# Kernel optimization log

Hardware: AMD Instinct MI355X
Metric: run time of the kernel (lower is better)

## Reference

```python
import jax, jax.numpy as jnp
import numpy as np

NV, NK, DK, DV, KC = 32, 16, 128, 128, 4  # value heads, key heads, head dims, conv kernel
EPS = 1e-6


def setup_inputs() -> dict:
    key = jax.random.key(0)
    ks = jax.random.split(key, 10)
    B, T, D = 2, 4096, 2048
    key_dim, value_dim = NK * DK, NV * DV
    conv_dim = 2 * key_dim + value_dim
    s = 0.02
    return {
        "hidden_states": jax.random.normal(ks[0], (B, T, D), jnp.float32),
        "W_qkv": jax.random.normal(ks[1], (D, conv_dim), jnp.float32) * s,
        "W_z": jax.random.normal(ks[2], (D, value_dim), jnp.float32) * s,
        "W_b": jax.random.normal(ks[3], (D, NV), jnp.float32) * s,
        "W_a": jax.random.normal(ks[4], (D, NV), jnp.float32) * s,
        "conv_w": jax.random.normal(ks[5], (conv_dim, KC), jnp.float32) * 0.2,
        "dt_bias": jnp.ones((NV,), jnp.float32),
        "A_log": jnp.log(jax.random.uniform(ks[6], (NV,), jnp.float32, 0.5, 16.0)),
        "norm_w": jnp.ones((DV,), jnp.float32),
        "W_out": jax.random.normal(ks[7], (value_dim, D), jnp.float32) * s,
    }


def _silu(x):
    return x * jax.nn.sigmoid(x)


def _l2norm(x):
    return x * jax.lax.rsqrt(jnp.sum(x * x, axis=-1, keepdims=True) + EPS)


def _gated_delta_rule(q, k, v, g, beta):
    # q,k: [B,T,H,DK]; v: [B,T,H,DV]; g,beta: [B,T,H]
    tm = lambda x: jnp.moveaxis(x, 1, 0)  # time-major
    B, T, H = q.shape[0], q.shape[1], q.shape[2]
    S0 = jnp.zeros((B, H, q.shape[-1], v.shape[-1]), q.dtype)

    def step(S, xs):
        qt, kt, vt, gt, bt = xs
        S = S * jnp.exp(gt)[..., None, None]                       # decay
        kS = jnp.einsum('bhk,bhkv->bhv', kt, S)                    # k^T S
        S = S + bt[..., None, None] * kt[..., :, None] * (vt - kS)[..., None, :]
        o = jnp.einsum('bhk,bhkv->bhv', qt, S)
        return S, o

    _, o = jax.lax.scan(step, S0, (tm(q), tm(k), tm(v), tm(g), tm(beta)))
    return jnp.moveaxis(o, 0, 1)  # [B,T,H,DV]


def reference(hidden_states, W_qkv, W_z, W_b, W_a, conv_w, dt_bias, A_log, norm_w, W_out):
    B, T, D = hidden_states.shape
    key_dim, value_dim = NK * DK, NV * DV

    mixed = hidden_states @ W_qkv                                  # [B,T,conv_dim]
    z = (hidden_states @ W_z).reshape(B, T, NV, DV)
    beta = jax.nn.sigmoid(hidden_states @ W_b)                     # [B,T,NV]
    a = hidden_states @ W_a
    g = -jnp.exp(A_log) * jax.nn.softplus(a + dt_bias)             # [B,T,NV]

    # causal depthwise short conv (kernel KC) + silu
    xp = jnp.pad(mixed, ((0, 0), (KC - 1, 0), (0, 0)))
    conv = sum(xp[:, i:i + T, :] * conv_w[:, i] for i in range(KC))
    mixed = _silu(conv)

    q, k, v = jnp.split(mixed, [key_dim, 2 * key_dim], axis=-1)
    q = q.reshape(B, T, NK, DK)
    k = k.reshape(B, T, NK, DK)
    v = v.reshape(B, T, NV, DV)
    rep = NV // NK
    q = jnp.repeat(q, rep, axis=2)
    k = jnp.repeat(k, rep, axis=2)

    q = _l2norm(q) * (DK ** -0.5)
    k = _l2norm(k)

    o = _gated_delta_rule(q, k, v, g, beta)                        # [B,T,NV,DV]

    # fused gated RMSNorm: rmsnorm(o)*w * silu(z)
    var = jnp.mean(o * o, axis=-1, keepdims=True)
    o = o * jax.lax.rsqrt(var + 1e-6) * norm_w * _silu(z)

    return o.reshape(B, T, value_dim) @ W_out
```

## Files before the change

### kernel.cpp

```cpp
#include <hip/hip_runtime.h>
#include <hip/hip_bf16.h>


typedef __attribute__((ext_vector_type(8))) short short8;
typedef __attribute__((ext_vector_type(4))) float f32x4;
typedef unsigned short us;

static __device__ __forceinline__ us f2b(float f) {
  __hip_bfloat16 h = __float2bfloat16(f);
  return __builtin_bit_cast(us, h);
}
static __device__ __forceinline__ float b2f(us u) {
  return __bfloat162float(__builtin_bit_cast(__hip_bfloat16, u));
}

__global__ __launch_bounds__(256) void cvt_f32_bf16(const float* __restrict__ in,
    us* __restrict__ out, long n4) {
  long i = (long)blockIdx.x * 256 + threadIdx.x;
  long stride = (long)gridDim.x * 256;
  for (; i < n4; i += stride) {
    float4 f = reinterpret_cast<const float4*>(in)[i];
    ushort4 u;
    u.x = f2b(f.x); u.y = f2b(f.y); u.z = f2b(f.z); u.w = f2b(f.w);
    reinterpret_cast<ushort4*>(out)[i] = u;
  }
}

__global__ __launch_bounds__(256) void transpose_cvt(const float* __restrict__ in,
    us* __restrict__ out, int K, int N, int Nfull, int coloff, int row_off) {
  __shared__ float tile[64][65];
  int tid = threadIdx.x;
  int n0 = blockIdx.x * 64, k0 = blockIdx.y * 64;
  int tx = tid & 15, ty = tid >> 4;
#pragma unroll
  for (int r = 0; r < 4; ++r) {
    int kk = k0 + ty + r * 16, nn = n0 + tx * 4;
    float4 v = make_float4(0.f, 0.f, 0.f, 0.f);
    if (kk < K && nn < N)
      v = *reinterpret_cast<const float4*>(in + (size_t)kk * Nfull + coloff + nn);
    tile[ty + r * 16][tx * 4 + 0] = v.x;
    tile[ty + r * 16][tx * 4 + 1] = v.y;
    tile[ty + r * 16][tx * 4 + 2] = v.z;
    tile[ty + r * 16][tx * 4 + 3] = v.w;
  }
  __syncthreads();
#pragma unroll
  for (int g = 0; g < 2; ++g) {
    int s = tid + g * 256;
    int nn = s >> 3, ks = (s & 7) * 8;
    if (n0 + nn < N && k0 + ks < K) {
      us ov[8];
#pragma unroll
      for (int i = 0; i < 8; ++i) ov[i] = f2b(tile[ks + i][nn]);
      *reinterpret_cast<uint4*>(out + (size_t)(n0 + nn + row_off) * K + k0 + ks) =
          *reinterpret_cast<uint4*>(ov);
    }
  }
}

template <bool BF16OUT>
__global__ __launch_bounds__(512, 1) void gemm256(const us* __restrict__ A,
    const us* __restrict__ B, void* __restrict__ Cout, int K, int ldC) {
  __shared__ us Abuf[2][256 * 64];
  __shared__ us Bbuf[2][256 * 64];
  int tid = threadIdx.x, w = tid >> 6, lane = tid & 63;
  int wr = w >> 2, wc = w & 3;
  int fr = lane & 15, j4 = lane >> 4;
  int lin = blockIdx.y * gridDim.x + blockIdx.x;
  int nwg = gridDim.x * gridDim.y;
  int wg = (lin & 7) * (nwg >> 3) + (lin >> 3);
  int bx = wg % gridDim.x, by = wg / gridDim.x;
  size_t bm = (size_t)bx * 256, bn = (size_t)by * 256;

  const us *aG[4], *bG[4];
  us *aL[2][4], *bL[2][4];
#pragma unroll
  for (int u = 0; u < 4; ++u) {
    int idx = u * 512 + tid;
    int row = idx >> 3, sl = idx & 7;
    int sg = (sl ^ (row & 7)) * 8;
    aG[u] = A + (bm + row) * K + sg;
    bG[u] = B + (bn + row) * K + sg;
    int lbase = (u * 64 + w * 8) * 64;
#pragma unroll
    for (int bf = 0; bf < 2; ++bf) {
      aL[bf][u] = &Abuf[bf][lbase];
      bL[bf][u] = &Bbuf[bf][lbase];
    }
  }

  f32x4 acc[8][4] = {};
#pragma unroll
  for (int u = 0; u < 4; ++u) {
    __builtin_amdgcn_global_load_lds((const void*)aG[u], (void*)aL[0][u], 16, 0, 0);
    __builtin_amdgcn_global_load_lds((const void*)bG[u], (void*)bL[0][u], 16, 0, 0);
  }
  __syncthreads();

  int nt = K >> 6;
  for (int t = 0; t < nt; ++t) {
    int cur = t & 1, nxt = cur ^ 1;
    const us* Ac = Abuf[cur];
    const us* Bc = Bbuf[cur];
    int kt1 = (t + 1) << 6;
    bool more = (t + 1 < nt);
#pragma unroll
    for (int q = 0; q < 4; ++q) {
      if (more) {
        __builtin_amdgcn_global_load_lds((const void*)(aG[q] + kt1), (void*)aL[nxt][q], 16, 0, 0);
        __builtin_amdgcn_global_load_lds((const void*)(bG[q] + kt1), (void*)bL[nxt][q], 16, 0, 0);
      }
      short8 a0[2], a1[2], bfv[4][2];
      int Ra0 = wr * 128 + 2 * q * 16 + fr;
      int Ra1 = Ra0 + 16;
#pragma unroll
      for (int ks = 0; ks < 2; ++ks) {
        a0[ks] = *reinterpret_cast<const short8*>(&Ac[Ra0 * 64 + (((ks * 4 + j4) ^ (Ra0 & 7)) * 8)]);
        a1[ks] = *reinterpret_cast<const short8*>(&Ac[Ra1 * 64 + (((ks * 4 + j4) ^ (Ra1 & 7)) * 8)]);
#pragma unroll
        for (int fj = 0; fj < 4; ++fj) {
          int Rb = wc * 64 + fj * 16 + fr;
          bfv[fj][ks] = *reinterpret_cast<const short8*>(&Bc[Rb * 64 + (((ks * 4 + j4) ^ (Rb & 7)) * 8)]);
        }
      }
      __builtin_amdgcn_s_setprio(1);
#pragma unroll
      for (int ks = 0; ks < 2; ++ks)
#pragma unroll
        for (int fj = 0; fj < 4; ++fj) {
          acc[2 * q][fj] = __builtin_amdgcn_mfma_f32_16x16x32_bf16(a0[ks], bfv[fj][ks], acc[2 * q][fj], 0, 0, 0);
          acc[2 * q + 1][fj] = __builtin_amdgcn_mfma_f32_16x16x32_bf16(a1[ks], bfv[fj][ks], acc[2 * q + 1][fj], 0, 0, 0);
        }
      __builtin_amdgcn_s_setprio(0);
    }
    __syncthreads();
  }
#pragma unroll
  for (int fi = 0; fi < 8; ++fi)
#pragma unroll
    for (int fj = 0; fj < 4; ++fj) {
      size_t col = bn + wc * 64 + fj * 16 + fr;
#pragma unroll
      for (int e = 0; e < 4; ++e) {
        size_t r = bm + wr * 128 + fi * 16 + j4 * 4 + e;
        size_t off = r * ldC + col;
        if (BF16OUT) reinterpret_cast<us*>(Cout)[off] = f2b(acc[fi][fj][e]);
        else reinterpret_cast<float*>(Cout)[off] = acc[fi][fj][e];
      }
    }
}

__global__ __launch_bounds__(256) void gemm_lds_f32(const us* __restrict__ A,
    const us* __restrict__ B, float* __restrict__ Cout,
    int K, int Nb1, int Nvalid, int ldC) {
  __shared__ us Ash[128 * 64];
  __shared__ us Bsh[128 * 64];
  int tid = threadIdx.x, w = tid >> 6, lane = tid & 63;
  int bm = blockIdx.x * 128, bn = blockIdx.y * 128;
  int wm = (w >> 1) * 64, wn = (w & 1) * 64;
  const us* aP[4]; const us* bP[4]; us* lA[4]; us* lB[4];
#pragma unroll
  for (int i = 0; i < 4; ++i) {
    int idx = i * 256 + tid;
    int row = idx >> 3;
    int sg = ((idx & 7) ^ (row & 7)) * 8;
    aP[i] = A + (size_t)(bm + row) * K + sg;
    int rb = bn + row; if (rb > Nb1) rb = Nb1;
    bP[i] = B + (size_t)rb * K + sg;
    lA[i] = &Ash[(i * 256 + w * 64) * 8];
    lB[i] = &Bsh[(i * 256 + w * 64) * 8];
  }
  f32x4 acc[4][4] = {};
  int fr = lane & 15, j = lane >> 4;
  for (int kt = 0; kt < K; kt += 64) {
#pragma unroll
    for (int i = 0; i < 4; ++i)
      __builtin_amdgcn_global_load_lds((const void*)(aP[i] + kt), (void*)lA[i], 16, 0, 0);
#pragma unroll
    for (int i = 0; i < 4; ++i)
      __builtin_amdgcn_global_load_lds((const void*)(bP[i] + kt), (void*)lB[i], 16, 0, 0);
    __syncthreads();
#pragma unroll
    for (int ks = 0; ks < 2; ++ks) {
      short8 af[4], bfr[4];
#pragma unroll
      for (int f = 0; f < 4; ++f) {
        int Ra = wm + f * 16 + fr;
        af[f] = *reinterpret_cast<const short8*>(&Ash[Ra * 64 + (((ks * 4 + j) ^ (Ra & 7)) * 8)]);
        int Rb = wn + f * 16 + fr;
        bfr[f] = *reinterpret_cast<const short8*>(&Bsh[Rb * 64 + (((ks * 4 + j) ^ (Rb & 7)) * 8)]);
      }
#pragma unroll
      for (int i = 0; i < 4; ++i)
#pragma unroll
        for (int jj = 0; jj < 4; ++jj)
          acc[i][jj] = __builtin_amdgcn_mfma_f32_16x16x32_bf16(af[i], bfr[jj], acc[i][jj], 0, 0, 0);
    }
    __syncthreads();
  }
#pragma unroll
  for (int i = 0; i < 4; ++i)
#pragma unroll
    for (int jj = 0; jj < 4; ++jj) {
      int c0 = bn + wn + jj * 16 + (lane & 15);
      if (c0 < Nvalid) {
#pragma unroll
        for (int e = 0; e < 4; ++e) {
          int r = bm + wm + i * 16 + (lane >> 4) * 4 + e;
          Cout[(size_t)r * ldC + c0] = acc[i][jj][e];
        }
      }
    }
}

template <int MODE>
__global__ __launch_bounds__(256) void conv_chunk(const us* __restrict__ mixed,
    const float* __restrict__ cw, us* __restrict__ outp, int headbase) {
  int bt = blockIdx.x, b = bt >> 12, t = bt & 4095, tid = threadIdx.x;
  int c0 = tid * 8;
  float wv[8][4];
#pragma unroll
  for (int jj = 0; jj < 8; ++jj) {
    float4 w4 = *reinterpret_cast<const float4*>(cw + (size_t)(c0 + jj) * 4);
    wv[jj][0] = w4.x; wv[jj][1] = w4.y; wv[jj][2] = w4.z; wv[jj][3] = w4.w;
  }
  float acc[8] = {};
#pragma unroll
  for (int i = 0; i < 4; ++i) {
    int tt = t - 3 + i;
    if (tt >= 0) {
      us r[8];
      *reinterpret_cast<uint4*>(r) = *reinterpret_cast<const uint4*>(
          mixed + ((size_t)(b * 4096 + tt)) * 2048 + c0);
#pragma unroll
      for (int jj = 0; jj < 8; ++jj) acc[jj] += b2f(r[jj]) * wv[jj][i];
    }
  }
  float x[8];
#pragma unroll
  for (int jj = 0; jj < 8; ++jj) x[jj] = acc[jj] / (1.f + __expf(-acc[jj]));
  us ov[8];
  if (MODE < 2) {
    float s2 = 0.f;
#pragma unroll
    for (int jj = 0; jj < 8; ++jj) s2 += x[jj] * x[jj];
#pragma unroll
    for (int m = 1; m < 16; m <<= 1) s2 += __shfl_xor(s2, m, 64);
    float rn = rsqrtf(s2 + 1e-6f) * (MODE == 0 ? 0.08838834764831845f : 1.f);
#pragma unroll
    for (int jj = 0; jj < 8; ++jj) ov[jj] = f2b(x[jj] * rn);
    int head = tid >> 4, d0 = c0 & 127;
    *reinterpret_cast<uint4*>(outp + ((size_t)bt * 16 + head) * 128 + d0) =
        *reinterpret_cast<uint4*>(ov);
  } else {
#pragma unroll
    for (int jj = 0; jj < 8; ++jj) ov[jj] = f2b(x[jj]);
    *reinterpret_cast<uint4*>(outp + ((size_t)bt * 32 + headbase + (c0 >> 7)) * 128 + (c0 & 127)) =
        *reinterpret_cast<uint4*>(ov);
  }
}

__global__ __launch_bounds__(256) void gates_cumsum(const float* __restrict__ ba,
    const float* __restrict__ dt_bias, const float* __restrict__ A_log,
    float* __restrict__ bl_g, float* __restrict__ beta_g) {
  int widx = blockIdx.x * 4 + (threadIdx.x >> 6);
  int lane = threadIdx.x & 63;
  int bh = widx >> 6, chunk = widx & 63;
  int b = bh >> 5, h = bh & 31;
  size_t btl = (size_t)b * 4096 + chunk * 64 + lane;
  float bv = ba[btl * 64 + h];
  float av = ba[btl * 64 + 32 + h];
  float beta = 1.f / (1.f + __expf(-bv));
  float xx = av + dt_bias[h];
  float sp = (xx > 20.f) ? xx : log1pf(__expf(xx));
  float g = -__expf(A_log[h]) * sp;
#pragma unroll
  for (int off = 1; off < 64; off <<= 1) {
    float n = __shfl_up(g, off, 64);
    if (lane >= off) g += n;
  }
  bl_g[(size_t)widx * 64 + lane] = g;
  beta_g[(size_t)widx * 64 + lane] = beta;
}

static __device__ __forceinline__ f32x4 tile_range(const us* A, int lda,
    const us* B, int ldb, int rt, int ct, int l0, int nk, int lane, f32x4 acc) {
  const us* ar = A + (rt * 16 + (lane & 15)) * lda + l0 * 16 + (lane >> 4) * 8;
  const us* br = B + (ct * 16 + (lane & 15)) * ldb + l0 * 16 + (lane >> 4) * 8;
#pragma unroll
  for (int ks = 0; ks < nk; ++ks) {
    short8 a = *reinterpret_cast<const short8*>(ar + ks * 32);
    short8 bb = *reinterpret_cast<const short8*>(br + ks * 32);
    acc = __builtin_amdgcn_mfma_f32_16x16x32_bf16(a, bb, acc, 0, 0, 0);
  }
  return acc;
}

__global__ __launch_bounds__(512, 1) void scan_p1(
    const us* __restrict__ k, const float* __restrict__ bl_g,
    const float* __restrict__ beta_g, us* __restrict__ Tg) {
  __shared__ us Kb[64 * 136];
  __shared__ us Ebt[64 * 72];
  __shared__ us W1[64 * 72], W1t[64 * 72], W3[64 * 72];
  __shared__ float bl_s[64], bet_s[64];
  us* const Eb = Kb;

  int bid = blockIdx.x, bh = bid >> 6, c = bid & 63;
  int b = bh >> 5, h = bh & 31, hk = h >> 1;
  int tid = threadIdx.x, w = tid >> 6, lane = tid & 63;
  int row = tid >> 3, c16 = (tid & 7) * 16;
  size_t bt0 = (size_t)b * 4096 + c * 64;

  const int TR_[10] = {0, 1, 1, 2, 2, 2, 3, 3, 3, 3};
  const int TC_[10] = {0, 0, 1, 0, 1, 2, 0, 1, 2, 3};

  const us* kp = k + ((bt0 + row) * 16 + hk) * 128 + c16;
  uint4 kr0 = reinterpret_cast<const uint4*>(kp)[0];
  uint4 kr1 = reinterpret_cast<const uint4*>(kp)[1];
  int gbase = (bh * 64 + c) * 64;
  if (tid < 64) { bl_s[tid] = bl_g[gbase + tid]; bet_s[tid] = beta_g[gbase + tid]; }
  *reinterpret_cast<uint4*>(&Kb[row * 136 + c16]) = kr0;
  *reinterpret_cast<uint4*>(&Kb[row * 136 + c16 + 8]) = kr1;
  __syncthreads();
  {
    int art = w & 3;
#pragma unroll
    for (int s = 0; s < 2; ++s) {
      int ct = (w >> 2) * 2 + s;
      f32x4 a = tile_range(Kb, 136, Kb, 136, art, ct, 0, 4, lane, f32x4{});
#pragma unroll
      for (int e = 0; e < 4; ++e) {
        int tr = art * 16 + (lane >> 4) * 4 + e;
        int cl = ct * 16 + (lane & 15);
        float dv = (cl < tr) ? bet_s[tr] * __expf(bl_s[tr] - bl_s[cl]) * a[e] : 0.f;
        W1[tr * 72 + cl] = f2b(dv);
        W1t[cl * 72 + tr] = f2b(dv);
        W3[tr * 72 + cl] = f2b((tr == cl ? 1.f : 0.f) - dv);
      }
    }
  }
  __syncthreads();
  f32x4 freg[2] = {};
#pragma unroll
  for (int it = 1; it <= 5; ++it) {
    if (it > 1) {
#pragma unroll
      for (int s = 0; s < 2; ++s) {
        int j = w + s * 8;
        if (j < 10) {
          int r = TR_[j], cc0 = TC_[j];
#pragma unroll
          for (int e = 0; e < 4; ++e) {
            int rr = r * 16 + (lane >> 4) * 4 + e, cl = cc0 * 16 + (lane & 15);
            W3[rr * 72 + cl] = f2b(b2f(W3[rr * 72 + cl]) + freg[s][e]);
          }
        }
      }
    }
    if (it == 1) {
      const int ZR[12] = {0, 0, 0, 1, 1, 2, 1, 2, 2, 3, 3, 3};
      const int ZC[12] = {1, 2, 3, 2, 3, 3, 0, 0, 1, 0, 1, 2};
#pragma unroll
      for (int u = 0; u < 12; ++u) {
        if ((u & 7) != w) continue;
        us* arr = (u < 6) ? Eb : Ebt;
        if (lane < 32) {
          int rr = ZR[u] * 16 + (lane >> 1);
          *reinterpret_cast<uint4*>(&arr[rr * 72 + ZC[u] * 16 + (lane & 1) * 8]) =
              make_uint4(0, 0, 0, 0);
        }
      }
    }
    const us* Es  = (it & 1) ? W1  : Eb;
    const us* Est = (it & 1) ? W1t : Ebt;
    us* Ed  = (it & 1) ? Eb  : W1;
    us* Edt = (it & 1) ? Ebt : W1t;
#pragma unroll
    for (int s = 0; s < 2; ++s) {
      int j = w + s * 8;
      if (j < 10) {
        int r = TR_[j], cc0 = TC_[j];
        int l0 = cc0 & ~1, nk = (r - l0 + 2) >> 1;
        f32x4 a = tile_range(Es, 72, Est, 72, r, cc0, l0, nk, lane, f32x4{});
#pragma unroll
        for (int e = 0; e < 4; ++e) {
          int rr = r * 16 + (lane >> 4) * 4 + e, cl = cc0 * 16 + (lane & 15);
          us val = f2b(a[e]);
          Ed[rr * 72 + cl] = val;
          Edt[cl * 72 + rr] = val;
        }
      }
    }
    __syncthreads();
    const us* Ent = (it & 1) ? Ebt : W1t;
#pragma unroll
    for (int s = 0; s < 2; ++s) {
      int j = w + s * 8;
      if (j < 10) {
        int r = TR_[j], cc0 = TC_[j];
        int l0 = cc0 & ~1, nk = (r - l0 + 2) >> 1;
        freg[s] = tile_range(W3, 72, Ent, 72, r, cc0, l0, nk, lane, f32x4{});
      }
    }
    __syncthreads();
  }
#pragma unroll
  for (int s = 0; s < 2; ++s) {
    int j = w + s * 8;
    if (j < 10) {
      int r = TR_[j], cc0 = TC_[j];
#pragma unroll
      for (int e = 0; e < 4; ++e) {
        int rr = r * 16 + (lane >> 4) * 4 + e, cl = cc0 * 16 + (lane & 15);
        W3[rr * 72 + cl] = f2b(b2f(W3[rr * 72 + cl]) + freg[s][e]);
      }
    }
  }
  __syncthreads();
  *reinterpret_cast<uint4*>(&Tg[(size_t)bid * 4096 + tid * 8]) =
      *reinterpret_cast<const uint4*>(&W3[row * 72 + (tid & 7) * 8]);
}

__global__ __launch_bounds__(512, 1) void scan_p2(
    const us* __restrict__ q, const us* __restrict__ k, const us* __restrict__ v,
    const float* __restrict__ bl_g, const float* __restrict__ beta_g,
    const us* __restrict__ Tg, us* __restrict__ o) {
  __shared__ us Sb[32 * 136];
  __shared__ us Kb[64 * 136];
  __shared__ us Qb[64 * 136];
  __shared__ us Ktb[128 * 72];
  __shared__ us Vt[32 * 72];
  __shared__ us Ut[32 * 72];
  __shared__ us W3[64 * 72];
  __shared__ us WP[64 * 72];
  __shared__ float bl_s[64], bet_s[64];

  int bid = blockIdx.x, vs = bid >> 6, bh = bid & 63;
  int b = bh >> 5, h = bh & 31, hk = h >> 1;
  int tid = threadIdx.x, w = tid >> 6, lane = tid & 63;
  int row = tid >> 3, c16 = (tid & 7) * 16;

  for (int i = tid; i < (32 * 136) / 8; i += 512)
    reinterpret_cast<uint4*>(Sb)[i] = make_uint4(0, 0, 0, 0);
  __syncthreads();

  uint4 kr0, kr1, qr0, qr1, vr, Tr;
  float blr, blC, bet, betv;
  int vrow = (tid & 255) >> 2, vseg = tid & 3;
  auto load_regs = [&](int c) {
    size_t bt0 = (size_t)b * 4096 + c * 64;
    const us* kp = k + ((bt0 + row) * 16 + hk) * 128 + c16;
    const us* qp = q + ((bt0 + row) * 16 + hk) * 128 + c16;
    kr0 = reinterpret_cast<const uint4*>(kp)[0];
    kr1 = reinterpret_cast<const uint4*>(kp)[1];
    qr0 = reinterpret_cast<const uint4*>(qp)[0];
    qr1 = reinterpret_cast<const uint4*>(qp)[1];
    Tr = *reinterpret_cast<const uint4*>(&Tg[((size_t)bh * 64 + c) * 4096 + tid * 8]);
    int gbase = (bh * 64 + c) * 64;
    blr = bl_g[gbase + row];
    blC = bl_g[gbase + 63];
    bet = beta_g[gbase + row];
    if (tid < 256) {
      vr = *reinterpret_cast<const uint4*>(
          v + ((bt0 + vrow) * 32 + h) * 128 + vs * 32 + vseg * 8);
      betv = beta_g[gbase + vrow];
    }
  };
  load_regs(0);

  for (int c = 0; c < 64; ++c) {
    size_t bt0 = (size_t)b * 4096 + c * 64;
    if ((tid & 7) == 0) { bl_s[row] = blr; bet_s[row] = bet; }
    *reinterpret_cast<uint4*>(&Kb[row * 136 + c16]) = kr0;
    *reinterpret_cast<uint4*>(&Kb[row * 136 + c16 + 8]) = kr1;
    *reinterpret_cast<uint4*>(&Qb[row * 136 + c16]) = qr0;
    *reinterpret_cast<uint4*>(&Qb[row * 136 + c16 + 8]) = qr1;
    *reinterpret_cast<uint4*>(&W3[row * 72 + (tid & 7) * 8]) = Tr;
    {
      us kreg[16];
      *reinterpret_cast<uint4*>(kreg) = kr0; *reinterpret_cast<uint4*>(kreg + 8) = kr1;
      float ksc = __expf(blC - blr);
#pragma unroll
      for (int i = 0; i < 16; ++i) Ktb[(c16 + i) * 72 + row] = f2b(ksc * b2f(kreg[i]));
    }
    if (tid < 256) {
      us vreg[8];
      *reinterpret_cast<uint4*>(vreg) = vr;
#pragma unroll
      for (int i = 0; i < 8; ++i) Vt[(vseg * 8 + i) * 72 + vrow] = f2b(betv * b2f(vreg[i]));
    }
    load_regs(c < 63 ? c + 1 : 63);
    __syncthreads();
    int rtO = w >> 1, ctv = w & 1;
    f32x4 o1 = tile_range(Qb, 136, Sb, 136, rtO, ctv, 0, 4, lane, f32x4{});
    {
      int art = w & 3;
#pragma unroll
      for (int s = 0; s < 2; ++s) {
        int ct = (w >> 2) * 2 + s;
        f32x4 a = tile_range(Qb, 136, Kb, 136, art, ct, 0, 4, lane, f32x4{});
#pragma unroll
        for (int e = 0; e < 4; ++e) {
          int tr = art * 16 + (lane >> 4) * 4 + e;
          int cl = ct * 16 + (lane & 15);
          float pv = (cl <= tr) ? __expf(bl_s[tr] - bl_s[cl]) * a[e] : 0.f;
          WP[tr * 72 + cl] = f2b(pv);
        }
      }
    }
    {
      int vrt = w >> 2, ct = w & 3;
      f32x4 a = tile_range(Sb, 136, Kb, 136, vrt, ct, 0, 4, lane, f32x4{});
      int tt = ct * 16 + (lane & 15);
      float csc = bet_s[tt] * __expf(bl_s[tt]);
#pragma unroll
      for (int e = 0; e < 4; ++e) {
        int vv = vrt * 16 + (lane >> 4) * 4 + e;
        Vt[vv * 72 + tt] = f2b(b2f(Vt[vv * 72 + tt]) - csc * a[e]);
      }
    }
    __syncthreads();
    {
      int vrt = w >> 2, ct = w & 3;
      f32x4 a = tile_range(Vt, 72, W3, 72, vrt, ct, 0, 2, lane, f32x4{});
#pragma unroll
      for (int e = 0; e < 4; ++e)
        Ut[(vrt * 16 + (lane >> 4) * 4 + e) * 72 + ct * 16 + (lane & 15)] = f2b(a[e]);
    }
    __syncthreads();
    float lamC = __expf(bl_s[63]);
    {
      f32x4 a = tile_range(WP, 72, Ut, 72, rtO, ctv, 0, 2, lane, f32x4{});
#pragma unroll
      for (int e = 0; e < 4; ++e) {
        int tt = rtO * 16 + (lane >> 4) * 4 + e;
        int vv = vs * 32 + ctv * 16 + (lane & 15);
        float val = __expf(bl_s[tt]) * o1[e] + a[e];
        o[((bt0 + tt) * 32 + h) * 128 + vv] = f2b(val);
      }
    }
#pragma unroll
    for (int s = 0; s < 2; ++s) {
      int ti = w * 2 + s;
      int vrt = ti >> 3, dt = ti & 7;
      f32x4 a = tile_range(Ut, 72, Ktb, 72, vrt, dt, 0, 2, lane, f32x4{});
#pragma unroll
      for (int e = 0; e < 4; ++e) {
        int vv = vrt * 16 + (lane >> 4) * 4 + e, dd = dt * 16 + (lane & 15);
        Sb[vv * 136 + dd] = f2b(lamC * b2f(Sb[vv * 136 + dd]) + a[e]);
      }
    }
    __syncthreads();
  }
}

__global__ __launch_bounds__(256) void rms_gate(us* oy,
    const us* __restrict__ z, const float* __restrict__ nw) {
  int sub = threadIdx.x & 31;
  size_t row = (size_t)blockIdx.x * 8 + (threadIdx.x >> 5);
  size_t base = row * 128 + sub * 4;
  ushort4 ov = *reinterpret_cast<ushort4*>(oy + base);
  ushort4 zv = *reinterpret_cast<const ushort4*>(z + base);
  float o_[4] = {b2f(ov.x), b2f(ov.y), b2f(ov.z), b2f(ov.w)};
  float ss = o_[0] * o_[0] + o_[1] * o_[1] + o_[2] * o_[2] + o_[3] * o_[3];
#pragma unroll
  for (int m = 1; m < 32; m <<= 1) ss += __shfl_xor(ss, m, 64);
  float r = rsqrtf(ss * (1.f / 128.f) + 1e-6f);
  float4 w4 = *reinterpret_cast<const float4*>(nw + sub * 4);
  float zz[4] = {b2f(zv.x), b2f(zv.y), b2f(zv.z), b2f(zv.w)};
  float wv[4] = {w4.x, w4.y, w4.z, w4.w};
  us res[4];
#pragma unroll
  for (int i = 0; i < 4; ++i) {
    float zs = zz[i] / (1.f + __expf(-zz[i]));
    res[i] = f2b(o_[i] * r * wv[i] * zs);
  }
  *reinterpret_cast<ushort4*>(oy + base) = *reinterpret_cast<ushort4*>(res);
}

extern "C" void kernel_launch(void* const* d_in, const int* in_sizes, int n_in,
                              void* d_out, int out_size, void* d_ws, size_t ws_size,
                              hipStream_t stream) {
  const float* hs      = (const float*)d_in[0];
  const float* W_qkv   = (const float*)d_in[1];
  const float* W_z     = (const float*)d_in[2];
  const float* W_b     = (const float*)d_in[3];
  const float* W_a     = (const float*)d_in[4];
  const float* conv_w  = (const float*)d_in[5];
  const float* dt_bias = (const float*)d_in[6];
  const float* A_log   = (const float*)d_in[7];
  const float* norm_w  = (const float*)d_in[8];
  const float* W_out   = (const float*)d_in[9];
  float* out = (float*)d_out;

  char* ws = (char*)d_ws;
  const size_t MiB = 1u << 20;
  float* ba_buf = (float*)(ws);
  float* bl_g   = (float*)(ws + 2 * MiB);
  float* bt_g   = (float*)(ws + 3 * MiB);
  us*    wt     = (us*)(ws + 4 * MiB);
  us*    Tg     = (us*)(ws + 4 * MiB);
  us*    mixed  = (us*)(ws + 36 * MiB);
  us*    o_buf  = (us*)(ws + 36 * MiB);
  us*    hs_bf0 = (us*)(ws + 68 * MiB);
  us*    q_buf  = (us*)(ws + 100 * MiB);
  us*    hs_bf1 = q_buf;
  us*    k_buf  = (us*)(ws + 132 * MiB);
  us*    v_buf  = (us*)(ws + 164 * MiB);
  us*    z_bf   = v_buf;

  cvt_f32_bf16<<<2048, 256, 0, stream>>>(hs, hs_bf0, (long)8192 * 2048 / 4);

  for (int c = 0; c < 4; ++c) {
    transpose_cvt<<<dim3(32, 32), 256, 0, stream>>>(W_qkv, wt, 2048, 2048, 8192, c * 2048, 0);
    gemm256<true><<<dim3(32, 8), 512, 0, stream>>>(hs_bf0, wt, mixed, 2048, 2048);
    const float* cwc = conv_w + (size_t)c * 2048 * 4;
    if (c == 0)      conv_chunk<0><<<8192, 256, 0, stream>>>(mixed, cwc, q_buf, 0);
    else if (c == 1) conv_chunk<1><<<8192, 256, 0, stream>>>(mixed, cwc, k_buf, 0);
    else if (c == 2) conv_chunk<2><<<8192, 256, 0, stream>>>(mixed, cwc, v_buf, 0);
    else             conv_chunk<2><<<8192, 256, 0, stream>>>(mixed, cwc, v_buf, 16);
  }
  transpose_cvt<<<dim3(1, 32), 256, 0, stream>>>(W_b, wt, 2048, 32, 32, 0, 0);
  transpose_cvt<<<dim3(1, 32), 256, 0, stream>>>(W_a, wt, 2048, 32, 32, 0, 32);
  gemm_lds_f32<<<dim3(64, 1), 256, 0, stream>>>(hs_bf0, wt, ba_buf, 2048, 63, 64, 64);
  gates_cumsum<<<1024, 256, 0, stream>>>(ba_buf, dt_bias, A_log, bl_g, bt_g);
  scan_p1<<<4096, 512, 0, stream>>>(k_buf, bl_g, bt_g, Tg);
  scan_p2<<<256, 512, 0, stream>>>(q_buf, k_buf, v_buf, bl_g, bt_g, Tg, o_buf);
  cvt_f32_bf16<<<2048, 256, 0, stream>>>(hs, hs_bf1, (long)8192 * 2048 / 4);
  transpose_cvt<<<dim3(64, 32), 256, 0, stream>>>(W_z, wt, 2048, 4096, 4096, 0, 0);
  gemm256<true><<<dim3(32, 16), 512, 0, stream>>>(hs_bf1, wt, z_bf, 2048, 4096);
  rms_gate<<<32768, 256, 0, stream>>>(o_buf, z_bf, norm_w);
  transpose_cvt<<<dim3(32, 64), 256, 0, stream>>>(W_out, wt, 4096, 2048, 2048, 0, 0);
  gemm256<false><<<dim3(32, 8), 512, 0, stream>>>(o_buf, wt, out, 4096, 2048);
}
```

Measured before the change: 1.250 ms.

## Split scan_p2 value dimension into 16-wide slices across twice the blocks

The chunked delta-rule scan kernel now gives each block a 16-column slice of the value dimension instead of 32, and launches 512 blocks instead of 256. The state, V and U tiles in shared memory shrink to match, and the per-wave work assignment is changed so half the waves handle the state/U path and half the output path. The goal is more parallelism on the GPU for the sequential scan. The cost is that each block recomputes the Q·K and decay-mask tiles and reloads the Q/K/T data for a smaller slice, and some waves sit idle in several phases.

```diff
diff --git a/kernel.cpp b/kernel.cpp
--- a/kernel.cpp
+++ b/kernel.cpp
@@ -425,12 +425,12 @@
     const us* __restrict__ q, const us* __restrict__ k, const us* __restrict__ v,
     const float* __restrict__ bl_g, const float* __restrict__ beta_g,
     const us* __restrict__ Tg, us* __restrict__ o) {
-  __shared__ us Sb[32 * 136];
+  __shared__ us Sb[16 * 136];
   __shared__ us Kb[64 * 136];
   __shared__ us Qb[64 * 136];
   __shared__ us Ktb[128 * 72];
-  __shared__ us Vt[32 * 72];
-  __shared__ us Ut[32 * 72];
+  __shared__ us Vt[16 * 72];
+  __shared__ us Ut[16 * 72];
   __shared__ us W3[64 * 72];
   __shared__ us WP[64 * 72];
   __shared__ float bl_s[64], bet_s[64];
@@ -440,13 +440,13 @@
   int tid = threadIdx.x, w = tid >> 6, lane = tid & 63;
   int row = tid >> 3, c16 = (tid & 7) * 16;
 
-  for (int i = tid; i < (32 * 136) / 8; i += 512)
+  for (int i = tid; i < (16 * 136) / 8; i += 512)
     reinterpret_cast<uint4*>(Sb)[i] = make_uint4(0, 0, 0, 0);
   __syncthreads();
 
   uint4 kr0, kr1, qr0, qr1, vr, Tr;
   float blr, blC, bet, betv;
-  int vrow = (tid & 255) >> 2, vseg = tid & 3;
+  int vrow = (tid & 127) >> 1, vseg = tid & 1;
   auto load_regs = [&](int c) {
     size_t bt0 = (size_t)b * 4096 + c * 64;
     const us* kp = k + ((bt0 + row) * 16 + hk) * 128 + c16;
@@ -460,9 +460,9 @@
     blr = bl_g[gbase + row];
     blC = bl_g[gbase + 63];
     bet = beta_g[gbase + row];
-    if (tid < 256) {
+    if (tid < 128) {
       vr = *reinterpret_cast<const uint4*>(
-          v + ((bt0 + vrow) * 32 + h) * 128 + vs * 32 + vseg * 8);
+          v + ((bt0 + vrow) * 32 + h) * 128 + vs * 16 + vseg * 8);
       betv = beta_g[gbase + vrow];
     }
   };
@@ -483,7 +483,7 @@
 #pragma unroll
       for (int i = 0; i < 16; ++i) Ktb[(c16 + i) * 72 + row] = f2b(ksc * b2f(kreg[i]));
     }
-    if (tid < 256) {
+    if (tid < 128) {
       us vreg[8];
       *reinterpret_cast<uint4*>(vreg) = vr;
 #pragma unroll
@@ -491,8 +491,9 @@
     }
     load_regs(c < 63 ? c + 1 : 63);
     __syncthreads();
-    int rtO = w >> 1, ctv = w & 1;
-    f32x4 o1 = tile_range(Qb, 136, Sb, 136, rtO, ctv, 0, 4, lane, f32x4{});
+    f32x4 o1 = {};
+    if (w >= 4)
+      o1 = tile_range(Qb, 136, Sb, 136, w - 4, 0, 0, 4, lane, f32x4{});
     {
       int art = w & 3;
 #pragma unroll
@@ -508,45 +509,41 @@
         }
       }
     }
-    {
-      int vrt = w >> 2, ct = w & 3;
-      f32x4 a = tile_range(Sb, 136, Kb, 136, vrt, ct, 0, 4, lane, f32x4{});
-      int tt = ct * 16 + (lane & 15);
+    if (w < 4) {
+      f32x4 a = tile_range(Sb, 136, Kb, 136, 0, w, 0, 4, lane, f32x4{});
+      int tt = w * 16 + (lane & 15);
       float csc = bet_s[tt] * __expf(bl_s[tt]);
 #pragma unroll
       for (int e = 0; e < 4; ++e) {
-        int vv = vrt * 16 + (lane >> 4) * 4 + e;
+        int vv = (lane >> 4) * 4 + e;
         Vt[vv * 72 + tt] = f2b(b2f(Vt[vv * 72 + tt]) - csc * a[e]);
       }
     }
     __syncthreads();
-    {
-      int vrt = w >> 2, ct = w & 3;
-      f32x4 a = tile_range(Vt, 72, W3, 72, vrt, ct, 0, 2, lane, f32x4{});
+    if (w < 4) {
+      f32x4 a = tile_range(Vt, 72, W3, 72, 0, w, 0, 2, lane, f32x4{});
 #pragma unroll
       for (int e = 0; e < 4; ++e)
-        Ut[(vrt * 16 + (lane >> 4) * 4 + e) * 72 + ct * 16 + (lane & 15)] = f2b(a[e]);
+        Ut[((lane >> 4) * 4 + e) * 72 + w * 16 + (lane & 15)] = f2b(a[e]);
     }
     __syncthreads();
     float lamC = __expf(bl_s[63]);
-    {
-      f32x4 a = tile_range(WP, 72, Ut, 72, rtO, ctv, 0, 2, lane, f32x4{});
+    if (w >= 4) {
+      int rtO = w - 4;
+      f32x4 a = tile_range(WP, 72, Ut, 72, rtO, 0, 0, 2, lane, f32x4{});
 #pragma unroll
       for (int e = 0; e < 4; ++e) {
         int tt = rtO * 16 + (lane >> 4) * 4 + e;
-        int vv = vs * 32 + ctv * 16 + (lane & 15);
+        int vv = vs * 16 + (lane & 15);
         float val = __expf(bl_s[tt]) * o1[e] + a[e];
         o[((bt0 + tt) * 32 + h) * 128 + vv] = f2b(val);
       }
     }
-#pragma unroll
-    for (int s = 0; s < 2; ++s) {
-      int ti = w * 2 + s;
-      int vrt = ti >> 3, dt = ti & 7;
-      f32x4 a = tile_range(Ut, 72, Ktb, 72, vrt, dt, 0, 2, lane, f32x4{});
+    {
+      f32x4 a = tile_range(Ut, 72, Ktb, 72, 0, w, 0, 2, lane, f32x4{});
 #pragma unroll
       for (int e = 0; e < 4; ++e) {
-        int vv = vrt * 16 + (lane >> 4) * 4 + e, dd = dt * 16 + (lane & 15);
+        int vv = (lane >> 4) * 4 + e, dd = w * 16 + (lane & 15);
         Sb[vv * 136 + dd] = f2b(lamC * b2f(Sb[vv * 136 + dd]) + a[e]);
       }
     }
@@ -625,7 +622,7 @@
   gemm_lds_f32<<<dim3(64, 1), 256, 0, stream>>>(hs_bf0, wt, ba_buf, 2048, 63, 64, 64);
   gates_cumsum<<<1024, 256, 0, stream>>>(ba_buf, dt_bias, A_log, bl_g, bt_g);
   scan_p1<<<4096, 512, 0, stream>>>(k_buf, bl_g, bt_g, Tg);
-  scan_p2<<<256, 512, 0, stream>>>(q_buf, k_buf, v_buf, bl_g, bt_g, Tg, o_buf);
+  scan_p2<<<512, 512, 0, stream>>>(q_buf, k_buf, v_buf, bl_g, bt_g, Tg, o_buf);
   cvt_f32_bf16<<<2048, 256, 0, stream>>>(hs, hs_bf1, (long)8192 * 2048 / 4);
   transpose_cvt<<<dim3(64, 32), 256, 0, stream>>>(W_z, wt, 2048, 4096, 4096, 0, 0);
   gemm256<true><<<dim3(32, 16), 512, 0, stream>>>(hs_bf1, wt, z_bf, 2048, 4096);
```

New measurement: 1.341 ms. +7.3%, slower.
